# Optimization experiments

Measured on AMD Instinct MI355X. Metric: run time of the kernel, lower is better.

## Reference

```python
import jax, jax.numpy as jnp
import numpy as np

NUM_USERS = 100000
NUM_ITEMS = 50000
EMB = 64
N_EDGES = 4800000
N_NODES = NUM_USERS + NUM_ITEMS
NEG_SLOPE = 0.01  # torch F.leaky_relu default


def setup_inputs() -> dict:
    key = jax.random.key(0)
    ks = jax.random.split(key, 12)
    inp = {
        "user_indices": jnp.arange(NUM_USERS, dtype=jnp.int32),
        "item_indices": jnp.arange(NUM_ITEMS, dtype=jnp.int32),
        "adj_rows": jax.random.randint(ks[0], (N_EDGES,), 0, N_NODES, dtype=jnp.int32),
        "adj_cols": jax.random.randint(ks[1], (N_EDGES,), 0, N_NODES, dtype=jnp.int32),
        "adj_vals": jax.random.uniform(ks[2], (N_EDGES,), dtype=jnp.float32),
        "user_emb": jax.random.normal(ks[3], (NUM_USERS, EMB), dtype=jnp.float32),
        "item_emb": jax.random.normal(ks[4], (NUM_ITEMS, EMB), dtype=jnp.float32),
    }
    # two propagation layers (layers=[64,64,64] -> zip gives 2 Linear pairs)
    s = 1.0 / np.sqrt(EMB)
    for li, kb in zip(range(2), range(5, 12, 4)):
        inp[f"W_gc{li}"] = jax.random.uniform(ks[kb], (EMB, EMB), jnp.float32, -s, s)
        inp[f"b_gc{li}"] = jax.random.uniform(ks[kb + 1], (EMB,), jnp.float32, -s, s)
        inp[f"W_bi{li}"] = jax.random.uniform(ks[kb + 2], (EMB, EMB), jnp.float32, -s, s)
        inp[f"b_bi{li}"] = jax.random.uniform(ks[kb + 3], (EMB,), jnp.float32, -s, s)
    return inp


def reference(user_indices, item_indices, adj_rows, adj_cols, adj_vals,
              user_emb, item_emb,
              W_gc0, b_gc0, W_bi0, b_bi0,
              W_gc1, b_gc1, W_bi1, b_bi1):
    ego = jnp.concatenate([user_emb[user_indices], item_emb[item_indices]], axis=0)  # [N, 64]
    n_nodes = ego.shape[0]
    all_embeddings = [ego]
    layer_params = [(W_gc0, b_gc0, W_bi0, b_bi0), (W_gc1, b_gc1, W_bi1, b_bi1)]
    for Wg, bg, Wb, bb in layer_params:
        # sparse adj @ ego : gather by col, scale by val, scatter-add by row
        side = jax.ops.segment_sum(adj_vals[:, None] * ego[adj_cols], adj_rows,
                                   num_segments=n_nodes)  # [N, 64]
        sum_emb = jax.nn.leaky_relu(side @ Wg.T + bg, NEG_SLOPE)
        bi_emb = jax.nn.leaky_relu((ego * side) @ Wb.T + bb, NEG_SLOPE)
        ego = sum_emb + bi_emb
        all_embeddings.append(ego)
    all_embeddings = jnp.concatenate(all_embeddings, axis=1)  # [N, 192]
    n_users = user_indices.shape[0]
    return all_embeddings[:n_users], all_embeddings[n_users:]
```

## Files before the change

kernel.cpp:

```cpp
#include <hip/hip_runtime.h>

#define NUSERS 100000
#define NITEMS 50000
#define NNODES 150000
#define EMB 64
#define NEDGES 4800000
#define OUTC 192
#define NEG_SLOPE 0.01f

#define BKT_SHIFT 10
#define NB 147
#define G 1024
#define EPB 4688
#define NSCAN (NB * G)

typedef __attribute__((ext_vector_type(8))) short bf16x8;
typedef __attribute__((ext_vector_type(4))) float f32x4;

__device__ __forceinline__ unsigned short f2bf(float f) {
    unsigned u = __float_as_uint(f);
    unsigned r = (u + 0x7fffu + ((u >> 16) & 1u)) >> 16;
    return (unsigned short)r;
}
__device__ __forceinline__ float bf2f(short s) {
    return __uint_as_float(((unsigned)(unsigned short)s) << 16);
}

__global__ void build_ego(const int* __restrict__ ui, const int* __restrict__ ii,
                          const float* __restrict__ uemb, const float* __restrict__ iemb,
                          float* __restrict__ out) {
    int gid = blockIdx.x * blockDim.x + threadIdx.x;
    int r = gid >> 4, p = gid & 15;
    if (r >= NNODES) return;
    const float* src = (r < NUSERS) ? (uemb + (size_t)ui[r] * EMB)
                                    : (iemb + (size_t)ii[r - NUSERS] * EMB);
    float4 v = ((const float4*)src)[p];
    *(float4*)(out + (size_t)r * OUTC + p * 4) = v;
}

__global__ void conv_bf16(const float* __restrict__ src, unsigned short* __restrict__ dst) {
    int gid = blockIdx.x * blockDim.x + threadIdx.x;
    int r = gid >> 4, p = gid & 15;
    if (r >= NNODES) return;
    float4 v = *(const float4*)(src + (size_t)r * OUTC + p * 4);
    ushort4 o;
    o.x = f2bf(v.x); o.y = f2bf(v.y); o.z = f2bf(v.z); o.w = f2bf(v.w);
    *(ushort4*)(dst + (size_t)r * EMB + p * 4) = o;
}

__global__ void conv_w(const float* __restrict__ s, unsigned short* __restrict__ d) {
    int i = blockIdx.x * 256 + threadIdx.x;
    if (i < 4096) d[i] = f2bf(s[i]);
}

__global__ __launch_bounds__(256) void bucket_hist(const int* __restrict__ rows,
                                                   int* __restrict__ hist) {
    __shared__ int h[NB];
    int tid = threadIdx.x, blk = blockIdx.x;
    if (tid < NB) h[tid] = 0;
    __syncthreads();
    int e0 = blk * EPB, e1 = e0 + EPB; if (e1 > NEDGES) e1 = NEDGES;
    for (int e = e0 + tid; e < e1; e += 256)
        atomicAdd(&h[rows[e] >> BKT_SHIFT], 1);
    __syncthreads();
    if (tid < NB) hist[(size_t)tid * G + blk] = h[tid];
}

__global__ void scan_chunk(const int* __restrict__ counts, int* __restrict__ outp,
                           int* __restrict__ blksum, int n) {
    __shared__ int buf[1024];
    int tid = threadIdx.x;
    int gid = blockIdx.x * 1024 + tid;
    int v = (gid < n) ? counts[gid] : 0;
    buf[tid] = v;
    __syncthreads();
    for (int off = 1; off < 1024; off <<= 1) {
        int t = (tid >= off) ? buf[tid - off] : 0;
        __syncthreads();
        buf[tid] += t;
        __syncthreads();
    }
    if (gid < n) outp[gid + 1] = buf[tid];
    if (tid == 1023) blksum[blockIdx.x] = buf[tid];
}

__global__ void scan_sums(int* __restrict__ blksum, int n) {
    __shared__ int buf[256];
    int tid = threadIdx.x;
    int v = (tid < n) ? blksum[tid] : 0;
    buf[tid] = v;
    __syncthreads();
    for (int off = 1; off < 256; off <<= 1) {
        int t = (tid >= off) ? buf[tid - off] : 0;
        __syncthreads();
        buf[tid] += t;
        __syncthreads();
    }
    if (tid < n) blksum[tid] = buf[tid] - v;
}

__global__ void add_offsets(int* __restrict__ outp, const int* __restrict__ blksum, int n) {
    int gid = blockIdx.x * 1024 + threadIdx.x;
    if (gid < n) outp[gid + 1] += blksum[blockIdx.x];
    if (gid == 0) outp[0] = 0;
}

__global__ __launch_bounds__(256) void bucket_scatter(
        const int* __restrict__ rows, const int* __restrict__ cols,
        const float* __restrict__ vals, const int* __restrict__ base,
        int2* __restrict__ bedge) {
    __shared__ int cur[NB];
    int tid = threadIdx.x, blk = blockIdx.x;
    if (tid < NB) cur[tid] = base[(size_t)tid * G + blk];
    __syncthreads();
    int e0 = blk * EPB, e1 = e0 + EPB; if (e1 > NEDGES) e1 = NEDGES;
    for (int e = e0 + tid; e < e1; e += 256) {
        int r = rows[e];
        int slot = atomicAdd(&cur[r >> BKT_SHIFT], 1);
        bedge[slot] = make_int2(cols[e] | ((r & 1023) << 18),
                                __float_as_int(vals[e]));
    }
}

__global__ __launch_bounds__(1024) void bucket_csr(
        const int2* __restrict__ bedge, const int* __restrict__ base,
        int* __restrict__ rowptr, int2* __restrict__ csr) {
    __shared__ int h[1024];
    __shared__ int h2[1024];
    int tid = threadIdx.x, bkt = blockIdx.x;
    int s  = base[(size_t)bkt * G];
    int e2 = base[(size_t)(bkt + 1) * G];
    h[tid] = 0;
    __syncthreads();
    for (int i = s + tid; i < e2; i += 1024)
        atomicAdd(&h[(unsigned)bedge[i].x >> 18], 1);
    __syncthreads();
    int v = h[tid];
    h2[tid] = v;
    __syncthreads();
    for (int off = 1; off < 1024; off <<= 1) {
        int t = (tid >= off) ? h2[tid - off] : 0;
        __syncthreads();
        h2[tid] += t;
        __syncthreads();
    }
    int excl = s + h2[tid] - v;
    int rbase = bkt << BKT_SHIFT;
    if (rbase + tid < NNODES) rowptr[rbase + tid] = excl;
    if (bkt == NB - 1 && tid == 0) rowptr[NNODES] = NEDGES;
    h[tid] = excl;
    __syncthreads();
    for (int i = s + tid; i < e2; i += 1024) {
        int2 t = bedge[i];
        int slot = atomicAdd(&h[(unsigned)t.x >> 18], 1);
        csr[slot] = make_int2(t.x & 0x3FFFF, t.y);
    }
}

#define ACC8(g, v)                                              \
    a0 = fmaf(v, __uint_as_float((g).x << 16), a0);             \
    a1 = fmaf(v, __uint_as_float((g).x & 0xffff0000u), a1);     \
    a2 = fmaf(v, __uint_as_float((g).y << 16), a2);             \
    a3 = fmaf(v, __uint_as_float((g).y & 0xffff0000u), a3);     \
    a4 = fmaf(v, __uint_as_float((g).z << 16), a4);             \
    a5 = fmaf(v, __uint_as_float((g).z & 0xffff0000u), a5);     \
    a6 = fmaf(v, __uint_as_float((g).w << 16), a6);             \
    a7 = fmaf(v, __uint_as_float((g).w & 0xffff0000u), a7);

__global__ __launch_bounds__(512) void spmm_gather(
        const int* __restrict__ rowptr, const int2* __restrict__ csr,
        const unsigned short* __restrict__ egoc,
        unsigned short* __restrict__ sideb,
        int strideE) {
    int tid = blockIdx.x * blockDim.x + threadIdx.x;
    int row = tid >> 3;
    int dg  = tid & 7;
    if (row >= NNODES) return;
    int s = rowptr[row], e = rowptr[row + 1];
    const uint4* egc = (const uint4*)egoc;
    float a0 = 0.f, a1 = 0.f, a2 = 0.f, a3 = 0.f,
          a4 = 0.f, a5 = 0.f, a6 = 0.f, a7 = 0.f;
    for (int b = s; b < e; b += 4) {
        int i1 = b + 1 < e ? b + 1 : e - 1;
        int i2 = b + 2 < e ? b + 2 : e - 1;
        int i3 = b + 3 < e ? b + 3 : e - 1;
        int2 cv0 = csr[b], cv1 = csr[i1], cv2 = csr[i2], cv3 = csr[i3];
        float v0 = __int_as_float(cv0.y);
        float v1 = (b + 1 < e) ? __int_as_float(cv1.y) : 0.f;
        float v2 = (b + 2 < e) ? __int_as_float(cv2.y) : 0.f;
        float v3 = (b + 3 < e) ? __int_as_float(cv3.y) : 0.f;
        uint4 g0 = egc[(size_t)cv0.x * 8 + dg];
        uint4 g1 = egc[(size_t)cv1.x * 8 + dg];
        uint4 g2 = egc[(size_t)cv2.x * 8 + dg];
        uint4 g3 = egc[(size_t)cv3.x * 8 + dg];
        ACC8(g0, v0); ACC8(g1, v1); ACC8(g2, v2); ACC8(g3, v3);
    }
    uint p0 = (unsigned)f2bf(a0) | ((unsigned)f2bf(a1) << 16);
    uint p1 = (unsigned)f2bf(a2) | ((unsigned)f2bf(a3) << 16);
    uint p2 = (unsigned)f2bf(a4) | ((unsigned)f2bf(a5) << 16);
    uint p3 = (unsigned)f2bf(a6) | ((unsigned)f2bf(a7) << 16);
    uint4 st = make_uint4(p0, p1, p2, p3);
    *(uint4*)(sideb + (size_t)row * strideE + dg * 8) = st;
}

__global__ __launch_bounds__(256) void dense_mfma(
        const unsigned short* __restrict__ sideb, int sStrideE,
        const unsigned short* __restrict__ egoc,
        const unsigned short* __restrict__ wg,
        const unsigned short* __restrict__ wb,
        const float* __restrict__ bg, const float* __restrict__ bb,
        float* __restrict__ outCol,
        unsigned short* __restrict__ egocNew) {
    int lane = threadIdx.x & 63;
    int ct   = (threadIdx.x >> 6) * 16;
    int rtile = blockIdx.x * 16;
    int ar = lane & 15, kg = lane >> 4;
    bf16x8 sfrag[2], pfrag[2], wgf[2], wbf[2];
    #pragma unroll
    for (int t = 0; t < 2; ++t) {
        int koff = kg * 8 + 32 * t;
        bf16x8 sv = *(const bf16x8*)(sideb + (size_t)(rtile + ar) * sStrideE + koff);
        bf16x8 ev = *(const bf16x8*)(egoc  + (size_t)(rtile + ar) * EMB + koff);
        sfrag[t] = sv;
        bf16x8 pv;
        #pragma unroll
        for (int j = 0; j < 8; ++j)
            pv[j] = (short)f2bf(bf2f(sv[j]) * bf2f(ev[j]));
        pfrag[t] = pv;
        wgf[t] = *(const bf16x8*)(wg + (size_t)(ct + ar) * EMB + koff);
        wbf[t] = *(const bf16x8*)(wb + (size_t)(ct + ar) * EMB + koff);
    }
    f32x4 accg = {0.f, 0.f, 0.f, 0.f}, accb = {0.f, 0.f, 0.f, 0.f};
    accg = __builtin_amdgcn_mfma_f32_16x16x32_bf16(sfrag[0], wgf[0], accg, 0, 0, 0);
    accg = __builtin_amdgcn_mfma_f32_16x16x32_bf16(sfrag[1], wgf[1], accg, 0, 0, 0);
    accb = __builtin_amdgcn_mfma_f32_16x16x32_bf16(pfrag[0], wbf[0], accb, 0, 0, 0);
    accb = __builtin_amdgcn_mfma_f32_16x16x32_bf16(pfrag[1], wbf[1], accb, 0, 0, 0);
    int c = ct + ar;
    float biasg = bg[c], biasb = bb[c];
    #pragma unroll
    for (int i = 0; i < 4; ++i) {
        int r = rtile + kg * 4 + i;
        float g = accg[i] + biasg; g = (g > 0.f) ? g : NEG_SLOPE * g;
        float q = accb[i] + biasb; q = (q > 0.f) ? q : NEG_SLOPE * q;
        float nv = g + q;
        outCol[(size_t)r * OUTC + c] = nv;
        if (egocNew) egocNew[(size_t)r * EMB + c] = f2bf(nv);
    }
}

extern "C" void kernel_launch(void* const* d_in, const int* in_sizes, int n_in,
                              void* d_out, int out_size, void* d_ws, size_t ws_size,
                              hipStream_t stream) {
    const int*   ui   = (const int*)  d_in[0];
    const int*   ii   = (const int*)  d_in[1];
    const int*   rows = (const int*)  d_in[2];
    const int*   cols = (const int*)  d_in[3];
    const float* vals = (const float*)d_in[4];
    const float* uemb = (const float*)d_in[5];
    const float* iemb = (const float*)d_in[6];
    const float* Wg0 = (const float*)d_in[7],  *bg0 = (const float*)d_in[8];
    const float* Wb0 = (const float*)d_in[9],  *bb0 = (const float*)d_in[10];
    const float* Wg1 = (const float*)d_in[11], *bg1 = (const float*)d_in[12];
    const float* Wb1 = (const float*)d_in[13], *bb1 = (const float*)d_in[14];
    float* out = (float*)d_out;

    char* ws = (char*)d_ws;
    int2*  csr    = (int2*)ws; ws += (size_t)NEDGES * 8;
    char*  buf0   = ws;        ws += (size_t)NNODES * EMB * 2;
    char*  buf1   = ws;        ws += (size_t)NNODES * EMB * 2;
    int*   rowptr = (int*) ws; ws += (size_t)(NNODES + 1) * 4;
    int*   hist   = (int*) ws; ws += (size_t)NSCAN * 4;
    int*   scanb  = (int*) ws; ws += (size_t)(NSCAN + 1) * 4;
    int*   blksum = (int*) ws; ws += 256 * 4;
    unsigned short* wgb0 = (unsigned short*)ws; ws += 4096 * 2;
    unsigned short* wbb0 = (unsigned short*)ws; ws += 4096 * 2;
    unsigned short* wgb1 = (unsigned short*)ws; ws += 4096 * 2;
    unsigned short* wbb1 = (unsigned short*)ws; ws += 4096 * 2;
    int2* bedge = (int2*)buf0;
    unsigned short* egoc0 = (unsigned short*)buf0;
    unsigned short* egoc1 = (unsigned short*)buf1;

    build_ego<<<(NNODES * 16 + 255) / 256, 256, 0, stream>>>(ui, ii, uemb, iemb, out);

    bucket_hist<<<G, 256, 0, stream>>>(rows, hist);
    scan_chunk<<<NSCAN / 1024, 1024, 0, stream>>>(hist, scanb, blksum, NSCAN);
    scan_sums<<<1, 256, 0, stream>>>(blksum, NSCAN / 1024);
    add_offsets<<<NSCAN / 1024, 1024, 0, stream>>>(scanb, blksum, NSCAN);
    bucket_scatter<<<G, 256, 0, stream>>>(rows, cols, vals, scanb, bedge);
    bucket_csr<<<NB, 1024, 0, stream>>>(bedge, scanb, rowptr, csr);

    conv_bf16<<<(NNODES * 16 + 255) / 256, 256, 0, stream>>>(out + 0, egoc0);
    conv_w<<<16, 256, 0, stream>>>(Wg0, wgb0);
    conv_w<<<16, 256, 0, stream>>>(Wb0, wbb0);
    conv_w<<<16, 256, 0, stream>>>(Wg1, wgb1);
    conv_w<<<16, 256, 0, stream>>>(Wb1, wbb1);

    unsigned short* side0 = (unsigned short*)((char*)out + 512);
    const int SIDE0_STRIDE = 384;
    spmm_gather<<<(NNODES * 8 + 511) / 512, 512, 0, stream>>>(rowptr, csr, egoc0,
                                                              side0, SIDE0_STRIDE);
    dense_mfma<<<NNODES / 16, 256, 0, stream>>>(side0, SIDE0_STRIDE, egoc0,
                                                wgb0, wbb0, bg0, bb0,
                                                out + 64, egoc1);

    unsigned short* side1 = (unsigned short*)buf0;
    spmm_gather<<<(NNODES * 8 + 511) / 512, 512, 0, stream>>>(rowptr, csr, egoc1,
                                                              side1, EMB);
    dense_mfma<<<NNODES / 16, 256, 0, stream>>>(side1, EMB, egoc1,
                                                wgb1, wbb1, bg1, bb1,
                                                out + 128, (unsigned short*)nullptr);
}
```

Measured before the change: 436.3 us.

## Fuse bf16 conversions into build_ego, vectorize bucketing loads, shuffle-share CSR in SpMM

The bf16 copy of the ego embeddings is now written directly by build_ego into a dedicated workspace buffer, and the four weight conversions are merged into one launch. This removes a re-read of the fp32 output and four small launches. The histogram and scatter kernels now read rows, cols and vals with 128-bit vector loads. In the SpMM, each lane of an 8-lane group loads one CSR entry and broadcasts it with shuffles, so a group handles 8 edges per iteration instead of loading every entry redundantly. The cost is an extra workspace buffer and more live registers in the gather loop.

```diff
diff --git a/kernel.cpp b/kernel.cpp
--- a/kernel.cpp
+++ b/kernel.cpp
@@ -28,7 +28,7 @@
 
 __global__ void build_ego(const int* __restrict__ ui, const int* __restrict__ ii,
                           const float* __restrict__ uemb, const float* __restrict__ iemb,
-                          float* __restrict__ out) {
+                          float* __restrict__ out, unsigned short* __restrict__ egoc) {
     int gid = blockIdx.x * blockDim.x + threadIdx.x;
     int r = gid >> 4, p = gid & 15;
     if (r >= NNODES) return;
@@ -36,21 +36,20 @@
                                     : (iemb + (size_t)ii[r - NUSERS] * EMB);
     float4 v = ((const float4*)src)[p];
     *(float4*)(out + (size_t)r * OUTC + p * 4) = v;
-}
-
-__global__ void conv_bf16(const float* __restrict__ src, unsigned short* __restrict__ dst) {
-    int gid = blockIdx.x * blockDim.x + threadIdx.x;
-    int r = gid >> 4, p = gid & 15;
-    if (r >= NNODES) return;
-    float4 v = *(const float4*)(src + (size_t)r * OUTC + p * 4);
     ushort4 o;
     o.x = f2bf(v.x); o.y = f2bf(v.y); o.z = f2bf(v.z); o.w = f2bf(v.w);
-    *(ushort4*)(dst + (size_t)r * EMB + p * 4) = o;
-}
-
-__global__ void conv_w(const float* __restrict__ s, unsigned short* __restrict__ d) {
+    *(ushort4*)(egoc + (size_t)r * EMB + p * 4) = o;
+}
+
+__global__ void conv_w4(const float* __restrict__ s0, const float* __restrict__ s1,
+                        const float* __restrict__ s2, const float* __restrict__ s3,
+                        unsigned short* __restrict__ d0, unsigned short* __restrict__ d1,
+                        unsigned short* __restrict__ d2, unsigned short* __restrict__ d3) {
     int i = blockIdx.x * 256 + threadIdx.x;
-    if (i < 4096) d[i] = f2bf(s[i]);
+    if (i < 4096) {
+        d0[i] = f2bf(s0[i]); d1[i] = f2bf(s1[i]);
+        d2[i] = f2bf(s2[i]); d3[i] = f2bf(s3[i]);
+    }
 }
 
 __global__ __launch_bounds__(256) void bucket_hist(const int* __restrict__ rows,
@@ -59,9 +58,16 @@
     int tid = threadIdx.x, blk = blockIdx.x;
     if (tid < NB) h[tid] = 0;
     __syncthreads();
-    int e0 = blk * EPB, e1 = e0 + EPB; if (e1 > NEDGES) e1 = NEDGES;
-    for (int e = e0 + tid; e < e1; e += 256)
-        atomicAdd(&h[rows[e] >> BKT_SHIFT], 1);
+    int q0 = blk * (EPB / 4), q1 = q0 + (EPB / 4);
+    const int qmax = NEDGES / 4;
+    if (q1 > qmax) q1 = qmax;
+    for (int q = q0 + tid; q < q1; q += 256) {
+        int4 r4 = ((const int4*)rows)[q];
+        atomicAdd(&h[r4.x >> BKT_SHIFT], 1);
+        atomicAdd(&h[r4.y >> BKT_SHIFT], 1);
+        atomicAdd(&h[r4.z >> BKT_SHIFT], 1);
+        atomicAdd(&h[r4.w >> BKT_SHIFT], 1);
+    }
     __syncthreads();
     if (tid < NB) hist[(size_t)tid * G + blk] = h[tid];
 }
@@ -113,12 +119,21 @@
     int tid = threadIdx.x, blk = blockIdx.x;
     if (tid < NB) cur[tid] = base[(size_t)tid * G + blk];
     __syncthreads();
-    int e0 = blk * EPB, e1 = e0 + EPB; if (e1 > NEDGES) e1 = NEDGES;
-    for (int e = e0 + tid; e < e1; e += 256) {
-        int r = rows[e];
-        int slot = atomicAdd(&cur[r >> BKT_SHIFT], 1);
-        bedge[slot] = make_int2(cols[e] | ((r & 1023) << 18),
-                                __float_as_int(vals[e]));
+    int q0 = blk * (EPB / 4), q1 = q0 + (EPB / 4);
+    const int qmax = NEDGES / 4;
+    if (q1 > qmax) q1 = qmax;
+    for (int q = q0 + tid; q < q1; q += 256) {
+        int4   r4 = ((const int4*)rows)[q];
+        int4   c4 = ((const int4*)cols)[q];
+        float4 v4 = ((const float4*)vals)[q];
+        int s0 = atomicAdd(&cur[r4.x >> BKT_SHIFT], 1);
+        bedge[s0] = make_int2(c4.x | ((r4.x & 1023) << 18), __float_as_int(v4.x));
+        int s1 = atomicAdd(&cur[r4.y >> BKT_SHIFT], 1);
+        bedge[s1] = make_int2(c4.y | ((r4.y & 1023) << 18), __float_as_int(v4.y));
+        int s2 = atomicAdd(&cur[r4.z >> BKT_SHIFT], 1);
+        bedge[s2] = make_int2(c4.z | ((r4.z & 1023) << 18), __float_as_int(v4.z));
+        int s3 = atomicAdd(&cur[r4.w >> BKT_SHIFT], 1);
+        bedge[s3] = make_int2(c4.w | ((r4.w & 1023) << 18), __float_as_int(v4.w));
     }
 }
 
@@ -176,24 +191,34 @@
     int row = tid >> 3;
     int dg  = tid & 7;
     if (row >= NNODES) return;
+    int lane = threadIdx.x & 63;
+    int g0l  = lane & ~7;
     int s = rowptr[row], e = rowptr[row + 1];
     const uint4* egc = (const uint4*)egoc;
     float a0 = 0.f, a1 = 0.f, a2 = 0.f, a3 = 0.f,
           a4 = 0.f, a5 = 0.f, a6 = 0.f, a7 = 0.f;
-    for (int b = s; b < e; b += 4) {
-        int i1 = b + 1 < e ? b + 1 : e - 1;
-        int i2 = b + 2 < e ? b + 2 : e - 1;
-        int i3 = b + 3 < e ? b + 3 : e - 1;
-        int2 cv0 = csr[b], cv1 = csr[i1], cv2 = csr[i2], cv3 = csr[i3];
-        float v0 = __int_as_float(cv0.y);
-        float v1 = (b + 1 < e) ? __int_as_float(cv1.y) : 0.f;
-        float v2 = (b + 2 < e) ? __int_as_float(cv2.y) : 0.f;
-        float v3 = (b + 3 < e) ? __int_as_float(cv3.y) : 0.f;
-        uint4 g0 = egc[(size_t)cv0.x * 8 + dg];
-        uint4 g1 = egc[(size_t)cv1.x * 8 + dg];
-        uint4 g2 = egc[(size_t)cv2.x * 8 + dg];
-        uint4 g3 = egc[(size_t)cv3.x * 8 + dg];
+    for (int b = s; b < e; b += 8) {
+        int idx = b + dg;
+        int2 cv = csr[idx < e ? idx : (e - 1)];
+        float vv = (idx < e) ? __int_as_float(cv.y) : 0.f;
+        int   c0 = __shfl(cv.x, g0l + 0); float v0 = __shfl(vv, g0l + 0);
+        int   c1 = __shfl(cv.x, g0l + 1); float v1 = __shfl(vv, g0l + 1);
+        int   c2 = __shfl(cv.x, g0l + 2); float v2 = __shfl(vv, g0l + 2);
+        int   c3 = __shfl(cv.x, g0l + 3); float v3 = __shfl(vv, g0l + 3);
+        int   c4 = __shfl(cv.x, g0l + 4); float v4 = __shfl(vv, g0l + 4);
+        int   c5 = __shfl(cv.x, g0l + 5); float v5 = __shfl(vv, g0l + 5);
+        int   c6 = __shfl(cv.x, g0l + 6); float v6 = __shfl(vv, g0l + 6);
+        int   c7 = __shfl(cv.x, g0l + 7); float v7 = __shfl(vv, g0l + 7);
+        uint4 g0 = egc[(size_t)c0 * 8 + dg];
+        uint4 g1 = egc[(size_t)c1 * 8 + dg];
+        uint4 g2 = egc[(size_t)c2 * 8 + dg];
+        uint4 g3 = egc[(size_t)c3 * 8 + dg];
+        uint4 g4 = egc[(size_t)c4 * 8 + dg];
+        uint4 g5 = egc[(size_t)c5 * 8 + dg];
+        uint4 g6 = egc[(size_t)c6 * 8 + dg];
+        uint4 g7 = egc[(size_t)c7 * 8 + dg];
         ACC8(g0, v0); ACC8(g1, v1); ACC8(g2, v2); ACC8(g3, v3);
+        ACC8(g4, v4); ACC8(g5, v5); ACC8(g6, v6); ACC8(g7, v7);
     }
     uint p0 = (unsigned)f2bf(a0) | ((unsigned)f2bf(a1) << 16);
     uint p1 = (unsigned)f2bf(a2) | ((unsigned)f2bf(a3) << 16);
@@ -268,6 +293,7 @@
     int2*  csr    = (int2*)ws; ws += (size_t)NEDGES * 8;
     char*  buf0   = ws;        ws += (size_t)NNODES * EMB * 2;
     char*  buf1   = ws;        ws += (size_t)NNODES * EMB * 2;
+    unsigned short* egoc0 = (unsigned short*)ws; ws += (size_t)NNODES * EMB * 2;
     int*   rowptr = (int*) ws; ws += (size_t)(NNODES + 1) * 4;
     int*   hist   = (int*) ws; ws += (size_t)NSCAN * 4;
     int*   scanb  = (int*) ws; ws += (size_t)(NSCAN + 1) * 4;
@@ -277,10 +303,11 @@
     unsigned short* wgb1 = (unsigned short*)ws; ws += 4096 * 2;
     unsigned short* wbb1 = (unsigned short*)ws; ws += 4096 * 2;
     int2* bedge = (int2*)buf0;
-    unsigned short* egoc0 = (unsigned short*)buf0;
     unsigned short* egoc1 = (unsigned short*)buf1;
 
-    build_ego<<<(NNODES * 16 + 255) / 256, 256, 0, stream>>>(ui, ii, uemb, iemb, out);
+    build_ego<<<(NNODES * 16 + 255) / 256, 256, 0, stream>>>(ui, ii, uemb, iemb,
+                                                             out, egoc0);
+    conv_w4<<<16, 256, 0, stream>>>(Wg0, Wb0, Wg1, Wb1, wgb0, wbb0, wgb1, wbb1);
 
     bucket_hist<<<G, 256, 0, stream>>>(rows, hist);
     scan_chunk<<<NSCAN / 1024, 1024, 0, stream>>>(hist, scanb, blksum, NSCAN);
@@ -288,12 +315,6 @@
     add_offsets<<<NSCAN / 1024, 1024, 0, stream>>>(scanb, blksum, NSCAN);
     bucket_scatter<<<G, 256, 0, stream>>>(rows, cols, vals, scanb, bedge);
     bucket_csr<<<NB, 1024, 0, stream>>>(bedge, scanb, rowptr, csr);
-
-    conv_bf16<<<(NNODES * 16 + 255) / 256, 256, 0, stream>>>(out + 0, egoc0);
-    conv_w<<<16, 256, 0, stream>>>(Wg0, wgb0);
-    conv_w<<<16, 256, 0, stream>>>(Wb0, wbb0);
-    conv_w<<<16, 256, 0, stream>>>(Wg1, wgb1);
-    conv_w<<<16, 256, 0, stream>>>(Wb1, wbb1);
 
     unsigned short* side0 = (unsigned short*)((char*)out + 512);
     const int SIDE0_STRIDE = 384;
```

Measured after the change: 410.0 us. -6.0%, faster.
